# Kernel optimization log

Hardware: AMD Instinct MI355X
Metric: run time of the kernel (lower is better)

## Reference

```python
import jax, jax.numpy as jnp
import numpy as np

TAU = 0.1
K = 60.0
CHUNK = 64
B = 1024


def setup_inputs() -> dict:
    key = jax.random.key(0)
    k1, k2, k3, k4 = jax.random.split(key, 4)
    s_v = jax.random.normal(k1, (B, B), jnp.float32)
    s_l = jax.random.normal(k2, (B, B), jnp.float32)
    # class-label based positive/negative masks (typical metric-learning batch)
    labels = jax.random.randint(k3, (B,), 0, B // 8)
    pos_mask = labels[:, None] == labels[None, :]
    neg_mask = ~pos_mask
    w_v = jax.random.uniform(k4, (B, B), jnp.float32)
    w_l = 1.0 - w_v
    return dict(s_v=s_v, s_l=s_l, pos_mask=pos_mask, neg_mask=neg_mask, w_v=w_v, w_l=w_l)


def _soft_ranks(sim, pos_f, neg_f, tau=TAU, chunk=CHUNK):
    """Row-chunked differentiable soft ranks. sim/pos_f/neg_f: [B, B] float."""
    b = sim.shape[0]
    nc = b // chunk  # B divisible by chunk

    def body(args):
        cs, cp, cn = args                                   # [chunk, B] each
        # sig[c, k, j] = sigmoid((s_ck - s_cj) / tau)
        sig = jax.nn.sigmoid((cs[:, :, None] - cs[:, None, :]) / tau)
        rank_pos = 1.0 + jnp.einsum('ckj,ck->cj', sig, cn)  # count negatives above
        rank_neg = 1.0 + jnp.einsum('ckj,ck->cj', sig, cp)  # count positives above
        return rank_pos * cp + rank_neg * cn

    args = (sim.reshape(nc, chunk, b), pos_f.reshape(nc, chunk, b), neg_f.reshape(nc, chunk, b))
    return jax.lax.map(jax.checkpoint(body), args).reshape(b, b)


def reference(s_v, s_l, pos_mask, neg_mask, w_v, w_l):
    pos_f = pos_mask.astype(s_v.dtype)
    neg_f = neg_mask.astype(s_v.dtype)
    rank_v = _soft_ranks(s_v, pos_f, neg_f)
    rank_l = _soft_ranks(s_l, pos_f, neg_f)
    S_hat = (K + 1.0) * (w_v / (K + rank_v) + w_l / (K + rank_l))
    return S_hat
```

## Files before the change

kernel.cpp:

```cpp
#include <hip/hip_runtime.h>


#define NB 1024
#define CEXP 14.426950408889634f
#define SCL  0.000030517578125f
#define NBUK 128
#define BUK0 4.3f
#define BUKW 14.883720930f
#define DBUK 3
#define CHSZ 128
#define NJOB 32
#define MAXPOS 64
#define ECLMP 1e17f
#define CLMP3 3e11f

typedef __attribute__((ext_vector_type(2))) float f32x2;
typedef __attribute__((ext_vector_type(2))) int   i32x2;

__device__ __forceinline__ f32x2 pk_fma(f32x2 a, f32x2 b, f32x2 c) {
    f32x2 d;
    asm("v_pk_fma_f32 %0, %1, %2, %3" : "=v"(d) : "v"(a), "v"(b), "v"(c));
    return d;
}
__device__ __forceinline__ f32x2 pk_mul(f32x2 a, f32x2 b) {
    f32x2 d;
    asm("v_pk_mul_f32 %0, %1, %2" : "=v"(d) : "v"(a), "v"(b));
    return d;
}
__device__ __forceinline__ f32x2 pk_add(f32x2 a, f32x2 b) {
    f32x2 d;
    asm("v_pk_add_f32 %0, %1, %2" : "=v"(d) : "v"(a), "v"(b));
    return d;
}
__device__ __forceinline__ f32x2 pk_fma_sat_lo(f32x2 es, f32x2 rp, f32x2 scl) {
    f32x2 d;
    asm("v_pk_fma_f32 %0, %1, %2, %3 op_sel_hi:[1,0,1] clamp"
        : "=v"(d) : "v"(es), "v"(rp), "v"(scl));
    return d;
}
__device__ __forceinline__ f32x2 pk_fma_sat_hi(f32x2 es, f32x2 rp, f32x2 scl) {
    f32x2 d;
    asm("v_pk_fma_f32 %0, %1, %2, %3 op_sel:[0,1,0] clamp"
        : "=v"(d) : "v"(es), "v"(rp), "v"(scl));
    return d;
}

#define PKTREE(L2q, Es2, A2, SCL2, TWO2, M1C)                      \
    {                                                              \
        const f32x2 P0 = (L2q)[0], P1 = (L2q)[1];                  \
        const f32x2 P2 = (L2q)[2], P3 = (L2q)[3];                  \
        const f32x2 y1 = pk_fma_sat_lo((Es2), P0, (SCL2));         \
        const f32x2 y2 = pk_fma_sat_hi((Es2), P0, (SCL2));         \
        const f32x2 y3 = pk_fma_sat_lo((Es2), P1, (SCL2));         \
        const f32x2 y4 = pk_fma_sat_hi((Es2), P1, (SCL2));         \
        const f32x2 y5 = pk_fma_sat_lo((Es2), P2, (SCL2));         \
        const f32x2 y6 = pk_fma_sat_hi((Es2), P2, (SCL2));         \
        const f32x2 y7 = pk_fma_sat_lo((Es2), P3, (SCL2));         \
        const f32x2 y8 = pk_fma_sat_hi((Es2), P3, (SCL2));         \
        const f32x2 p12 = pk_mul(y1, y2), p34 = pk_mul(y3, y4);    \
        const f32x2 p56 = pk_mul(y5, y6), p78 = pk_mul(y7, y8);    \
        const f32x2 s12 = pk_add(y1, y2), s34 = pk_add(y3, y4);    \
        const f32x2 s56 = pk_add(y5, y6), s78 = pk_add(y7, y8);    \
        const f32x2 q1 = pk_mul(p12, p34), q2 = pk_mul(p56, p78);  \
        const f32x2 n1 = pk_fma(s12, p34, pk_mul(s34, p12));       \
        const f32x2 n2 = pk_fma(s56, p78, pk_mul(s78, p56));       \
        const f32x2 num = pk_fma(n1, q2, pk_mul(n2, q1));          \
        const f32x2 den = pk_mul(q1, q2);                          \
        const i32x2 bi = 0x7EF311C3 - __builtin_bit_cast(i32x2, den); \
        f32x2 rr = __builtin_bit_cast(f32x2, bi);                  \
        const f32x2 dn = pk_mul(den, (M1C));                       \
        rr = pk_mul(rr, pk_fma(dn, rr, (TWO2)));                   \
        (A2) = pk_fma(num, rr, (A2));                              \
    }

__global__ __launch_bounds__(512) void drank_kernel(
    const float* __restrict__ s_v, const float* __restrict__ s_l,
    const unsigned char* __restrict__ pos_m,
    const unsigned char* __restrict__ neg_m,
    const float* __restrict__ w_v, const float* __restrict__ w_l,
    float* __restrict__ out)
{
    __shared__ __align__(16) float listRv[NB], listRl[NB];
    __shared__ unsigned char bktv[NB], bktl[NB];
    __shared__ unsigned short invv[NB], invl[NB];
    __shared__ float  sAv1[NB], sAv2[NB];
    __shared__ float  sAl1[NB], sAl2[NB];
    __shared__ int    offv[NBUK + 1], offl[NBUK + 1];
    __shared__ int    curv[NBUK], curl[NBUK];
    __shared__ float  SRv[129], SEv[129];
    __shared__ float  SR2v[129], SE2v[129];
    __shared__ float  SRl[129], SEl[129];
    __shared__ float  SR2l[129], SE2l[129];
    __shared__ float  SR3v[129], SE3v[129];
    __shared__ float  SR3l[129], SE3l[129];
    __shared__ float2 posR[MAXPOS];
    __shared__ int    npos_s, jobCtr;

    const int c = blockIdx.x;
    const int t = threadIdx.x;
    const long row = (long)c * NB;

    if (t < NBUK) { curv[t] = 0; curl[t] = 0; }
    if (t == 0) { npos_s = 0; jobCtr = 0; }
    __syncthreads();

    const unsigned int W =
        ((const unsigned int*)pos_m)[0] ^ ((const unsigned int*)neg_m)[0];
    const int mode = (W == 0x01010101u) ? 0 : ((W == 0x3f800000u) ? 2 : 1);

    const int j0 = t * 2;
    const float2 sjv = *(const float2*)(s_v + row + j0);
    const float2 sjl = *(const float2*)(s_l + row + j0);
    const float svu[2] = {sjv.x, sjv.y};
    const float slu[2] = {sjl.x, sjl.y};

    float Rv[2], Rl[2], Ev[2], El[2];
    int ibv[2], ibl[2];
    #pragma unroll
    for (int u = 0; u < 2; ++u) {
        Rv[u] = __builtin_amdgcn_exp2f(-svu[u] * CEXP);
        Rl[u] = __builtin_amdgcn_exp2f(-slu[u] * CEXP);
        Ev[u] = __builtin_amdgcn_exp2f(svu[u] * CEXP);
        El[u] = __builtin_amdgcn_exp2f(slu[u] * CEXP);
        ibv[u] = max(0, min(NBUK - 1, (int)((svu[u] + BUK0) * BUKW)));
        ibl[u] = max(0, min(NBUK - 1, (int)((slu[u] + BUK0) * BUKW)));
        atomicAdd(&curv[ibv[u]], 1);
        atomicAdd(&curl[ibl[u]], 1);
    }

    bool pj[2];
    if (mode == 0) {
        const unsigned short b = ((const unsigned short*)pos_m)[(row >> 1) + t];
        pj[0] = (b & 0x00ffu) != 0; pj[1] = (b & 0xff00u) != 0;
    } else if (mode == 2) {
        const float2 p = *(const float2*)((const float*)pos_m + row + j0);
        pj[0] = p.x != 0.f; pj[1] = p.y != 0.f;
    } else {
        const int2 p = *(const int2*)((const int*)pos_m + row + j0);
        pj[0] = p.x != 0; pj[1] = p.y != 0;
    }
    #pragma unroll
    for (int u = 0; u < 2; ++u) {
        if (pj[u]) {
            const int idx = atomicAdd(&npos_s, 1);
            if (idx < MAXPOS) posR[idx] = make_float2(Rv[u], Rl[u]);
        }
    }
    __syncthreads();

    if (t < 128) {
        const int m = t >> 6, l = t & 63;
        int* cnt = m ? curl : curv;
        int* off = m ? offl : offv;
        const int c0 = cnt[2 * l], c1 = cnt[2 * l + 1];
        int s = c0 + c1;
        #pragma unroll
        for (int d = 1; d < 64; d <<= 1) {
            const int y = __shfl_up(s, d, 64);
            if (l >= d) s += y;
        }
        const int excl = s - c0 - c1;
        off[2 * l] = excl;     off[2 * l + 1] = excl + c0;
        cnt[2 * l] = excl;     cnt[2 * l + 1] = excl + c0;
        if (l == 63) off[NBUK] = s;
    }
    __syncthreads();

    #pragma unroll
    for (int u = 0; u < 2; ++u) {
        const int pv = atomicAdd(&curv[ibv[u]], 1);
        listRv[pv] = Rv[u];
        bktv[pv]   = (unsigned char)ibv[u];
        invv[j0 + u] = (unsigned short)pv;
        const int pl = atomicAdd(&curl[ibl[u]], 1);
        listRl[pl] = Rl[u];
        bktl[pl]   = (unsigned char)ibl[u];
        invl[j0 + u] = (unsigned short)pl;
    }
    __syncthreads();

    {
        const int wid = t >> 6, l = t & 63;
        for (int f = wid; f < 12; f += 8) {
            const int m   = (f >> 1) & 1;
            const int fE  = f & 1;
            const int pw  = f >> 2;
            const float4* L4 = (const float4*)(m ? listRl : listRv);
            float* arr;
            switch (f) {
                case 0:  arr = SRv;  break;  case 1:  arr = SEv;  break;
                case 2:  arr = SRl;  break;  case 3:  arr = SEl;  break;
                case 4:  arr = SR2v; break;  case 5:  arr = SE2v; break;
                case 6:  arr = SR2l; break;  case 7:  arr = SE2l; break;
                case 8:  arr = SR3v; break;  case 9:  arr = SE3v; break;
                case 10: arr = SR3l; break;  default: arr = SE3l; break;
            }
            const int o0 = fE ? (2 * l) : (127 - 2 * l);
            const int o1 = fE ? (2 * l + 1) : (126 - 2 * l);
            float s01[2];
            #pragma unroll
            for (int q = 0; q < 2; ++q) {
                const int o = q ? o1 : o0;
                const float4 a = L4[2 * o], b = L4[2 * o + 1];
                float x[8] = {a.x, a.y, a.z, a.w, b.x, b.y, b.z, b.w};
                float acc = 0.f;
                #pragma unroll
                for (int i = 0; i < 8; ++i) {
                    const float v = fE ? __builtin_amdgcn_rcpf(x[i]) : x[i];
                    if (pw == 1) {
                        const float vc = fminf(v, ECLMP); acc += vc * vc;
                    } else if (pw == 2) {
                        const float vc = fminf(v, CLMP3); acc += vc * vc * vc;
                    } else {
                        acc += v;
                    }
                }
                s01[q] = acc;
            }
            float s = s01[0] + s01[1];
            #pragma unroll
            for (int d = 1; d < 64; d <<= 1) {
                const float y = __shfl_up(s, d, 64);
                if (l >= d) s += y;
            }
            if (fE) {
                const float excl = s - s01[0] - s01[1];
                arr[o0] = excl;  arr[o1] = excl + s01[0];
                if (l == 63) arr[128] = s;
            } else {
                arr[o1] = s;  arr[o0] = s - s01[1];
                if (l == 0) arr[128] = 0.f;
            }
        }
    }
    __syncthreads();

    static const unsigned char CORD[8] = {3, 4, 2, 5, 1, 6, 0, 7};
    const int lane = t & 63;
    const f32x2 SCL2 = {SCL, SCL};
    const f32x2 TWO2 = {2.0f, 2.0f};
    const f32x2 M1C  = {-1.0f, -1.0f};

    for (;;) {
        int jid0 = 0;
        if (lane == 0) jid0 = atomicAdd(&jobCtr, 1);
        const int jid = __builtin_amdgcn_readfirstlane(jid0);
        if (jid >= NJOB) break;
        const int ch = CORD[jid >> 2];
        const int m  = (jid >> 1) & 1;
        const int h  = jid & 1;

        const float* LR  = m ? listRl : listRv;
        const unsigned char* BK = m ? bktl : bktv;
        const int*   off = m ? offl : offv;
        float*       SA  = h ? (m ? sAl2 : sAv2) : (m ? sAl1 : sAv1);
        const float* SR  = m ? SRl : SRv;
        const float* SE  = m ? SEl : SEv;
        const float* SR2 = m ? SR2l : SR2v;
        const float* SE2 = m ? SE2l : SE2v;
        const float* SR3 = m ? SR3l : SR3v;
        const float* SE3 = m ? SE3l : SE3v;
        const f32x2* L2  = (const f32x2*)LR;

        const int p0 = ch * CHSZ + 2 * lane;
        const float2 R2 = *(const float2*)(LR + p0);
        const float Ex = __builtin_amdgcn_rcpf(R2.x);
        const float Ey = __builtin_amdgcn_rcpf(R2.y);
        const f32x2 Es2 = {SCL * Ex, SCL * Ey};

        const int bs = (int)BK[ch * CHSZ];
        const int be = (int)BK[ch * CHSZ + CHSZ - 1];
        const int lo0 = off[max(0, bs - DBUK)] & ~7;
        const int hi0 = (off[min(NBUK - 1, be + DBUK) + 1] + 7) & ~7;
        const int mid = ((lo0 + hi0) >> 1) & ~7;
        const int lo = h ? mid : lo0;
        const int hi = h ? hi0 : mid;

        f32x2 A2 = {0.f, 0.f};
        #pragma unroll 2
        for (int p = lo; p < hi; p += 8) {
            const f32x2* L2q = L2 + (p >> 1);
            PKTREE(L2q, Es2, A2, SCL2, TWO2, M1C);
        }
        float cx, cy;
        if (h) {
            const float sr = SR[hi0 >> 3], sr2 = SR2[hi0 >> 3], sr3 = SR3[hi0 >> 3];
            const float Exc = fminf(Ex, ECLMP), Eyc = fminf(Ey, ECLMP);
            const float Ex3 = fminf(Ex, CLMP3), Ey3 = fminf(Ey, CLMP3);
            cx = fmaf(Exc * Exc, sr2, (float)(NB - hi0) - Ex * sr)
                 - (Ex3 * Ex3 * Ex3) * sr3;
            cy = fmaf(Eyc * Eyc, sr2, (float)(NB - hi0) - Ey * sr)
                 - (Ey3 * Ey3 * Ey3) * sr3;
        } else {
            const float se = SE[lo0 >> 3], se2 = SE2[lo0 >> 3], se3 = SE3[lo0 >> 3];
            const float Rxc = fminf(R2.x, ECLMP), Ryc = fminf(R2.y, ECLMP);
            const float Rx3 = fminf(R2.x, CLMP3), Ry3 = fminf(R2.y, CLMP3);
            cx = fmaf(-(Rxc * Rxc), se2, R2.x * se)
                 + (Rx3 * Rx3 * Rx3) * se3;
            cy = fmaf(-(Ryc * Ryc), se2, R2.y * se)
                 + (Ry3 * Ry3 * Ry3) * se3;
        }
        float2 r;
        r.x = fmaf(A2.x, SCL, cx);
        r.y = fmaf(A2.y, SCL, cy);
        *(float2*)(SA + p0) = r;
    }

    float sPv[2] = {0.f, 0.f};
    float sPl[2] = {0.f, 0.f};
    const int np = min(npos_s, MAXPOS);
    for (int i = 0; i < np; ++i) {
        const float2 rp = posR[i];
        #pragma unroll
        for (int u = 0; u < 2; ++u) {
            sPv[u] += __builtin_amdgcn_rcpf(fmaf(Ev[u], rp.x, 1.0f));
            sPl[u] += __builtin_amdgcn_rcpf(fmaf(El[u], rp.y, 1.0f));
        }
    }
    __syncthreads();

    const int iv0 = invv[j0], iv1 = invv[j0 + 1];
    const int il0 = invl[j0], il1 = invl[j0 + 1];
    const float sAvu[2] = {sAv1[iv0] + sAv2[iv0], sAv1[iv1] + sAv2[iv1]};
    const float sAlu[2] = {sAl1[il0] + sAl2[il0], sAl1[il1] + sAl2[il1]};
    const float2 wv = *(const float2*)(w_v + row + j0);
    const float2 wl = *(const float2*)(w_l + row + j0);
    const float wva[2] = {wv.x, wv.y};
    const float wla[2] = {wl.x, wl.y};
    float o[2];
    #pragma unroll
    for (int u = 0; u < 2; ++u) {
        const float rv = pj[u] ? (1.0f + sAvu[u] - sPv[u]) : (1.0f + sPv[u]);
        const float rl = pj[u] ? (1.0f + sAlu[u] - sPl[u]) : (1.0f + sPl[u]);
        o[u] = 61.0f * (wva[u] / (60.0f + rv) + wla[u] / (60.0f + rl));
    }
    float2 o2;
    o2.x = o[0]; o2.y = o[1];
    *(float2*)(out + row + j0) = o2;
}

extern "C" void kernel_launch(void* const* d_in, const int* in_sizes, int n_in,
                              void* d_out, int out_size, void* d_ws, size_t ws_size,
                              hipStream_t stream) {
    const float* s_v = (const float*)d_in[0];
    const float* s_l = (const float*)d_in[1];
    const unsigned char* pos_m = (const unsigned char*)d_in[2];
    const unsigned char* neg_m = (const unsigned char*)d_in[3];
    const float* w_v = (const float*)d_in[4];
    const float* w_l = (const float*)d_in[5];
    float* out = (float*)d_out;

    drank_kernel<<<dim3(NB), dim3(512), 0, stream>>>(s_v, s_l, pos_m, neg_m, w_v, w_l, out);
}
```

Before: 122.5 us.

## Use per-lane bucket windows instead of per-chunk split halves

Each lane now computes its own exact-sum window from the buckets of its two elements, not a shared window spanning the whole 128-element chunk. This drops the two-half job split, so there are 16 jobs instead of 32, and removes the second set of sA arrays and the final add. Both tail corrections are now applied in a single job. Tighter windows cut the exact pairwise work, but lanes in a wave get different loop trip counts, which causes divergence, and there is less job-level parallelism across waves.

```diff
diff --git a/kernel.cpp b/kernel.cpp
--- a/kernel.cpp
+++ b/kernel.cpp
@@ -9,7 +9,7 @@
 #define BUKW 14.883720930f
 #define DBUK 3
 #define CHSZ 128
-#define NJOB 32
+#define NJOB 16
 #define MAXPOS 64
 #define ECLMP 1e17f
 #define CLMP3 3e11f
@@ -83,8 +83,7 @@
     __shared__ __align__(16) float listRv[NB], listRl[NB];
     __shared__ unsigned char bktv[NB], bktl[NB];
     __shared__ unsigned short invv[NB], invl[NB];
-    __shared__ float  sAv1[NB], sAv2[NB];
-    __shared__ float  sAl1[NB], sAl2[NB];
+    __shared__ float  sAv[NB], sAl[NB];
     __shared__ int    offv[NBUK + 1], offl[NBUK + 1];
     __shared__ int    curv[NBUK], curl[NBUK];
     __shared__ float  SRv[129], SEv[129];
@@ -246,14 +245,13 @@
         if (lane == 0) jid0 = atomicAdd(&jobCtr, 1);
         const int jid = __builtin_amdgcn_readfirstlane(jid0);
         if (jid >= NJOB) break;
-        const int ch = CORD[jid >> 2];
-        const int m  = (jid >> 1) & 1;
-        const int h  = jid & 1;
+        const int ch = CORD[jid >> 1];
+        const int m  = jid & 1;
 
         const float* LR  = m ? listRl : listRv;
         const unsigned char* BK = m ? bktl : bktv;
         const int*   off = m ? offl : offv;
-        float*       SA  = h ? (m ? sAl2 : sAv2) : (m ? sAl1 : sAv1);
+        float*       SA  = m ? sAl : sAv;
         const float* SR  = m ? SRl : SRv;
         const float* SE  = m ? SEl : SEv;
         const float* SR2 = m ? SR2l : SR2v;
@@ -268,38 +266,28 @@
         const float Ey = __builtin_amdgcn_rcpf(R2.y);
         const f32x2 Es2 = {SCL * Ex, SCL * Ey};
 
-        const int bs = (int)BK[ch * CHSZ];
-        const int be = (int)BK[ch * CHSZ + CHSZ - 1];
-        const int lo0 = off[max(0, bs - DBUK)] & ~7;
-        const int hi0 = (off[min(NBUK - 1, be + DBUK) + 1] + 7) & ~7;
-        const int mid = ((lo0 + hi0) >> 1) & ~7;
-        const int lo = h ? mid : lo0;
-        const int hi = h ? hi0 : mid;
+        const int b0 = (int)BK[p0];
+        const int b1 = (int)BK[p0 + 1];
+        const int lo = off[max(0, b0 - DBUK)] & ~7;
+        const int hi = (off[min(NBUK - 1, b1 + DBUK) + 1] + 7) & ~7;
 
         f32x2 A2 = {0.f, 0.f};
-        #pragma unroll 2
         for (int p = lo; p < hi; p += 8) {
             const f32x2* L2q = L2 + (p >> 1);
             PKTREE(L2q, Es2, A2, SCL2, TWO2, M1C);
         }
-        float cx, cy;
-        if (h) {
-            const float sr = SR[hi0 >> 3], sr2 = SR2[hi0 >> 3], sr3 = SR3[hi0 >> 3];
-            const float Exc = fminf(Ex, ECLMP), Eyc = fminf(Ey, ECLMP);
-            const float Ex3 = fminf(Ex, CLMP3), Ey3 = fminf(Ey, CLMP3);
-            cx = fmaf(Exc * Exc, sr2, (float)(NB - hi0) - Ex * sr)
-                 - (Ex3 * Ex3 * Ex3) * sr3;
-            cy = fmaf(Eyc * Eyc, sr2, (float)(NB - hi0) - Ey * sr)
-                 - (Ey3 * Ey3 * Ey3) * sr3;
-        } else {
-            const float se = SE[lo0 >> 3], se2 = SE2[lo0 >> 3], se3 = SE3[lo0 >> 3];
-            const float Rxc = fminf(R2.x, ECLMP), Ryc = fminf(R2.y, ECLMP);
-            const float Rx3 = fminf(R2.x, CLMP3), Ry3 = fminf(R2.y, CLMP3);
-            cx = fmaf(-(Rxc * Rxc), se2, R2.x * se)
-                 + (Rx3 * Rx3 * Rx3) * se3;
-            cy = fmaf(-(Ryc * Ryc), se2, R2.y * se)
-                 + (Ry3 * Ry3 * Ry3) * se3;
-        }
+        const float sr  = SR[hi >> 3], sr2 = SR2[hi >> 3], sr3 = SR3[hi >> 3];
+        const float se  = SE[lo >> 3], se2 = SE2[lo >> 3], se3 = SE3[lo >> 3];
+        const float cnt = (float)(NB - hi);
+        const float Exc = fminf(Ex, ECLMP),  Eyc = fminf(Ey, ECLMP);
+        const float Ex3 = fminf(Ex, CLMP3),  Ey3 = fminf(Ey, CLMP3);
+        const float Rxc = fminf(R2.x, ECLMP), Ryc = fminf(R2.y, ECLMP);
+        const float Rx3 = fminf(R2.x, CLMP3), Ry3 = fminf(R2.y, CLMP3);
+        float cx = fmaf(Exc * Exc, sr2, cnt - Ex * sr) - (Ex3 * Ex3 * Ex3) * sr3;
+        float cy = fmaf(Eyc * Eyc, sr2, cnt - Ey * sr) - (Ey3 * Ey3 * Ey3) * sr3;
+        cx += fmaf(-(Rxc * Rxc), se2, R2.x * se) + (Rx3 * Rx3 * Rx3) * se3;
+        cy += fmaf(-(Ryc * Ryc), se2, R2.y * se) + (Ry3 * Ry3 * Ry3) * se3;
+
         float2 r;
         r.x = fmaf(A2.x, SCL, cx);
         r.y = fmaf(A2.y, SCL, cy);
@@ -321,8 +309,8 @@
 
     const int iv0 = invv[j0], iv1 = invv[j0 + 1];
     const int il0 = invl[j0], il1 = invl[j0 + 1];
-    const float sAvu[2] = {sAv1[iv0] + sAv2[iv0], sAv1[iv1] + sAv2[iv1]};
-    const float sAlu[2] = {sAl1[il0] + sAl2[il0], sAl1[il1] + sAl2[il1]};
+    const float sAvu[2] = {sAv[iv0], sAv[iv1]};
+    const float sAlu[2] = {sAl[il0], sAl[il1]};
     const float2 wv = *(const float2*)(w_v + row + j0);
     const float2 wl = *(const float2*)(w_l + row + j0);
     const float wva[2] = {wv.x, wv.y};
```

Result: faster. 112.2 us (-8.4%).
